# Optimization experiments

Hardware: AMD Instinct MI355X
Metric: run time of the kernel (lower is better)

Reference implementation:

```python
import jax, jax.numpy as jnp
import numpy as np

N, E, H = 50000, 300000, 8  # nodes, edges, FeaStConv heads (PyG default)


def _lin_init(k, fan_in, fan_out):
    k1, k2 = jax.random.split(k)
    s = 1.0 / np.sqrt(fan_in)
    w = jax.random.uniform(k1, (fan_in, fan_out), jnp.float32, -s, s)
    b = jax.random.uniform(k2, (fan_out,), jnp.float32, -s, s)
    return w, b


def _conv_init(k, cin, cout):
    k1, k2 = jax.random.split(k)
    w = jax.random.normal(k1, (cin, H * cout), jnp.float32) * 0.1   # weight
    u = jax.random.normal(k2, (cin, H), jnp.float32) * 0.1          # attention u
    c = jnp.zeros((H,), jnp.float32)                                 # attention bias
    b = jnp.zeros((cout,), jnp.float32)                              # output bias
    return w, u, c, b


def setup_inputs() -> dict:
    key = jax.random.key(0)
    ks = jax.random.split(key, 10)
    x = jax.random.normal(ks[0], (N, 3), jnp.float32)
    src = jax.random.randint(ks[1], (E,), 0, N)
    dst = jax.random.randint(ks[2], (E,), 0, N)
    dst = jnp.where(src == dst, (dst + 1) % N, dst)  # no self loops in raw edge list
    edge_index = jnp.stack([src, dst]).astype(jnp.int64)
    labels = (jax.random.uniform(ks[3], (N, 1)) < 0.1).astype(jnp.float32)
    lin1_w, lin1_b = _lin_init(ks[4], 3, 16)
    c1_w, c1_u, c1_c, c1_b = _conv_init(ks[5], 16, 32)
    c2_w, c2_u, c2_c, c2_b = _conv_init(ks[6], 32, 64)
    c3_w, c3_u, c3_c, c3_b = _conv_init(ks[7], 64, 128)
    lin2_w, lin2_b = _lin_init(ks[8], 128, 1024)
    lin3_w, lin3_b = _lin_init(ks[9], 1024, 1)
    return dict(x=x, edge_index=edge_index, labels=labels,
                lin1_w=lin1_w, lin1_b=lin1_b,
                c1_w=c1_w, c1_u=c1_u, c1_c=c1_c, c1_b=c1_b,
                c2_w=c2_w, c2_u=c2_u, c2_c=c2_c, c2_b=c2_b,
                c3_w=c3_w, c3_u=c3_u, c3_c=c3_c, c3_b=c3_b,
                lin2_w=lin2_w, lin2_b=lin2_b, lin3_w=lin3_w, lin3_b=lin3_b)


def feast_conv(x, src, dst, W, u, c, b):
    """PyG FeaStConv: gather x_i/x_j, head-softmax attention on (x_j - x_i),
    per-edge weighted sum over heads, mean-scatter to destination nodes."""
    n = x.shape[0]
    loop = jnp.arange(n, dtype=src.dtype)
    s = jnp.concatenate([src, loop])  # add self loops (PyG default)
    d = jnp.concatenate([dst, loop])
    xi = x[d]
    xj = x[s]
    q = jax.nn.softmax((xj - xi) @ u + c, axis=-1)           # [E+N, H]
    m = (xj @ W).reshape(xj.shape[0], H, -1)                  # [E+N, H, O]
    msg = jnp.einsum('eh,eho->eo', q, m)                      # [E+N, O]
    agg = jax.ops.segment_sum(msg, d, num_segments=n)
    cnt = jax.ops.segment_sum(jnp.ones_like(d, dtype=msg.dtype), d, num_segments=n)
    return agg / cnt[:, None] + b                             # mean aggregation + bias


def reference(x, edge_index, labels,
              lin1_w, lin1_b,
              c1_w, c1_u, c1_c, c1_b,
              c2_w, c2_u, c2_c, c2_b,
              c3_w, c3_u, c3_c, c3_b,
              lin2_w, lin2_b, lin3_w, lin3_b):
    src, dst = edge_index[0], edge_index[1]
    h = jax.nn.relu(x @ lin1_w + lin1_b)
    h = jax.nn.relu(feast_conv(h, src, dst, c1_w, c1_u, c1_c, c1_b))
    h = jax.nn.relu(feast_conv(h, src, dst, c2_w, c2_u, c2_c, c2_b))
    h = jax.nn.relu(feast_conv(h, src, dst, c3_w, c3_u, c3_c, c3_b))
    h = jax.nn.relu(h @ lin2_w + lin2_b)
    p = jax.nn.sigmoid(h @ lin3_w + lin3_b)                   # [N, 1]
    # generate_weights: class-balanced per-element BCE weights
    n = labels.shape[0]
    pos = jnp.sum(labels)
    neg = n - pos
    w = jnp.where(labels == 1, n / (2.0 * pos), n / (2.0 * neg))
    # torch-style BCE with log clamped at -100
    bce = -(labels * jnp.clip(jnp.log(p), -100.0, None)
            + (1.0 - labels) * jnp.clip(jnp.log(1.0 - p), -100.0, None))
    loss = jnp.mean(w * bce)
    return loss, p
```

## Files before the change

### kernel.cpp

```cpp
#include <hip/hip_runtime.h>
#include <math.h>

#define NN 50000
#define NE 300000

typedef short s8v __attribute__((ext_vector_type(8)));
typedef float f4v __attribute__((ext_vector_type(4)));

__device__ inline unsigned short f2bf(float f) {
    union { float f; unsigned int u; } v; v.f = f;
    unsigned int r = v.u + 0x7FFFu + ((v.u >> 16) & 1u);
    return (unsigned short)(r >> 16);
}

template<int CIN, int O>
__device__ inline void packw_feast_body(const float* __restrict__ W,
                                        unsigned short* __restrict__ wp, int t) {
    constexpr int NS = (8*CIN) / 32;
    int l = t & 63;
    int s = (t >> 6) % NS;
    int ct = t / (64 * NS);
    int c = ct*16 + (l & 15);
    int kk0 = s*32 + (l >> 4) * 8;
    union { unsigned short u[8]; s8v v; } o;
    #pragma unroll
    for (int i = 0; i < 8; ++i) {
        int kk = kk0 + i;
        int h = kk / CIN, k = kk & (CIN - 1);
        o.u[i] = f2bf(W[(size_t)k*(8*O) + h*O + c]);
    }
    *(s8v*)(wp + (size_t)t*8) = o.v;
}

__device__ inline void packw_lin_body(const float* __restrict__ W,
                                      unsigned short* __restrict__ wp, int t) {
    int l = t & 63;
    int s = (t >> 6) & 3;
    int ctg = t >> 8;
    int c = ctg*16 + (l & 15);
    int k0 = s*32 + (l >> 4) * 8;
    union { unsigned short u[8]; s8v v; } o;
    #pragma unroll
    for (int i = 0; i < 8; ++i) o.u[i] = f2bf(W[(size_t)(k0+i)*1024 + c]);
    *(s8v*)(wp + (size_t)t*8) = o.v;
}

__global__ __launch_bounds__(256) void prep_kernel(
        const float* __restrict__ l2w, unsigned short* __restrict__ w2p,
        const float* __restrict__ wf1w, unsigned short* __restrict__ wf1,
        const float* __restrict__ wf2w, unsigned short* __restrict__ wf2,
        const float* __restrict__ wf3w, unsigned short* __restrict__ wf3,
        int* __restrict__ fill, int* __restrict__ fill2,
        float* __restrict__ z, float* __restrict__ scal,
        const float* __restrict__ x, const float* __restrict__ l1w,
        const float* __restrict__ l1b, const float* __restrict__ u1,
        float* __restrict__ h1, float* __restrict__ a) {
    __shared__ float hsh[16][16];
    int b = blockIdx.x;
    int tid = threadIdx.x;
    if (b < 64)  { packw_lin_body(l2w, w2p, b*256 + tid); return; }
    b -= 64;
    if (b < 2)   { packw_feast_body<16,32>(wf1w, wf1, b*256 + tid); return; }
    b -= 2;
    if (b < 8)   { packw_feast_body<32,64>(wf2w, wf2, b*256 + tid); return; }
    b -= 8;
    if (b < 32)  { packw_feast_body<64,128>(wf3w, wf3, b*256 + tid); return; }
    b -= 32;
    if (b < 587) {
        int idx = b*256 + tid;
        if (idx < NN)            fill[idx] = 0;
        else if (idx < 2*NN)     fill2[idx - NN] = 0;
        else if (idx < 3*NN)     z[idx - 2*NN] = 0.f;
        else if (idx < 3*NN+16)  scal[idx - 3*NN] = 0.f;
        return;
    }
    b -= 587;
    int n0 = b * 16;
    int node = n0 + (tid >> 4), col = tid & 15;
    float v = x[node*3+0]*l1w[col] + x[node*3+1]*l1w[16+col]
            + x[node*3+2]*l1w[32+col] + l1b[col];
    v = fmaxf(v, 0.f);
    h1[(size_t)node*16 + col] = v;
    hsh[tid >> 4][col] = v;
    __syncthreads();
    if (tid < 128) {
        int t2 = tid >> 3, h = tid & 7;
        float acc = 0.f;
        #pragma unroll
        for (int k = 0; k < 16; ++k) acc += hsh[t2][k] * u1[k*8 + h];
        a[(size_t)(n0 + t2)*8 + h] = acc;
    }
}

__global__ void hist_kernel(const int* __restrict__ dst, int* __restrict__ cnt) {
    int e = blockIdx.x * 256 + threadIdx.x;
    if (e < NE) atomicAdd(&cnt[dst[e]], 1);
}

__global__ void scan1_kernel(const int* __restrict__ cnt, int* __restrict__ rp,
                             int* __restrict__ bpart) {
    __shared__ int sh[256];
    int tid = threadIdx.x;
    int gid = blockIdx.x * 256 + tid;
    int v = (gid < NN) ? cnt[gid] : 0;
    sh[tid] = v;
    __syncthreads();
    for (int off = 1; off < 256; off <<= 1) {
        int t = (tid >= off) ? sh[tid - off] : 0;
        __syncthreads();
        sh[tid] += t;
        __syncthreads();
    }
    if (gid < NN) rp[gid] = sh[tid] - v;
    if (tid == 255) bpart[blockIdx.x] = sh[tid];
}

__global__ void scanfix_kernel(int* __restrict__ rp, const int* __restrict__ bpart,
                               int nblk) {
    __shared__ int sh[256];
    int tid = threadIdx.x;
    int bx = blockIdx.x;
    sh[tid] = (tid < bx && tid < nblk) ? bpart[tid] : 0;
    __syncthreads();
    for (int off = 128; off; off >>= 1) {
        if (tid < off) sh[tid] += sh[tid + off];
        __syncthreads();
    }
    int add = sh[0];
    int gid = bx * 256 + tid;
    if (gid < NN) rp[gid] += add;
    if (gid == 0) rp[NN] = NE;
}

__global__ void scatter_kernel(const int* __restrict__ src, const int* __restrict__ dst,
                               const int* __restrict__ rp, int* __restrict__ fill,
                               int* __restrict__ ssrc, int* __restrict__ sdst) {
    int e = blockIdx.x * 256 + threadIdx.x;
    if (e >= NE) return;
    int d = dst[e];
    int pos = rp[d] + atomicAdd(&fill[d], 1);
    ssrc[pos] = src[e];
    sdst[pos] = d;
}

__global__ void q_sorted_kernel(const int* __restrict__ ssrc,
                                const int* __restrict__ sdst,
                                const float* __restrict__ a,
                                const float* __restrict__ c,
                                float* __restrict__ qs) {
    int j = blockIdx.x * 256 + threadIdx.x;
    if (j >= NE) return;
    int s = ssrc[j], d = sdst[j];
    const float4* as = (const float4*)(a + (size_t)s*8);
    const float4* ad = (const float4*)(a + (size_t)d*8);
    float4 s0 = as[0], s1 = as[1], d0 = ad[0], d1 = ad[1];
    float lg[8] = { s0.x-d0.x+c[0], s0.y-d0.y+c[1], s0.z-d0.z+c[2], s0.w-d0.w+c[3],
                    s1.x-d1.x+c[4], s1.y-d1.y+c[5], s1.z-d1.z+c[6], s1.w-d1.w+c[7] };
    float m = lg[0];
    #pragma unroll
    for (int h = 1; h < 8; ++h) m = fmaxf(m, lg[h]);
    float sum = 0.f;
    #pragma unroll
    for (int h = 0; h < 8; ++h) { lg[h] = __expf(lg[h]-m); sum += lg[h]; }
    float inv = 1.f / sum;
    float4* qp = (float4*)(qs + (size_t)j*8);
    qp[0] = make_float4(lg[0]*inv, lg[1]*inv, lg[2]*inv, lg[3]*inv);
    qp[1] = make_float4(lg[4]*inv, lg[5]*inv, lg[6]*inv, lg[7]*inv);
}

template<int HPER>
__device__ inline void load_qv(const float* __restrict__ qs, int j, int hg, float* qv) {
    if constexpr (HPER == 2) {
        float2 t = *(const float2*)(qs + (size_t)j*8 + hg*2);
        qv[0] = t.x; qv[1] = t.y;
    } else if constexpr (HPER == 4) {
        float4 t = *(const float4*)(qs + (size_t)j*8 + hg*4);
        qv[0] = t.x; qv[1] = t.y; qv[2] = t.z; qv[3] = t.w;
    } else {
        float4 t0 = *(const float4*)(qs + (size_t)j*8);
        float4 t1 = *(const float4*)(qs + (size_t)j*8 + 4);
        qv[0] = t0.x; qv[1] = t0.y; qv[2] = t0.z; qv[3] = t0.w;
        qv[4] = t1.x; qv[5] = t1.y; qv[6] = t1.z; qv[7] = t1.w;
    }
}

template<int CIN>
__global__ __launch_bounds__(256) void agg_kernel(
        const float* __restrict__ hin, const float* __restrict__ cbias,
        const int* __restrict__ rowptr, const int* __restrict__ ssrc,
        const float* __restrict__ qs, unsigned short* __restrict__ g) {
    constexpr int HPER = CIN / 8;
    constexpr int LG = (CIN == 16) ? 4 : (CIN == 32) ? 5 : 6;
    const int lane = threadIdx.x & 63;
    const int d = blockIdx.x * 4 + (threadIdx.x >> 6);
    const int k = lane & (CIN - 1);
    const int hg = lane >> LG;
    float m = cbias[0];
    #pragma unroll
    for (int h = 1; h < 8; ++h) m = fmaxf(m, cbias[h]);
    float ssum = 0.f;
    #pragma unroll
    for (int h = 0; h < 8; ++h) ssum += __expf(cbias[h] - m);
    float sinv = 1.f / ssum;
    float xd = hin[(size_t)d*CIN + k];
    float acc[HPER];
    #pragma unroll
    for (int i = 0; i < HPER; ++i)
        acc[i] = __expf(cbias[hg*HPER + i] - m) * sinv * xd;
    int j0 = rowptr[d], j1 = rowptr[d+1];
    int j = j0;
    for (; j + 2 <= j1; j += 2) {
        int s0 = ssrc[j], s1 = ssrc[j+1];
        float xv0 = hin[(size_t)s0*CIN + k];
        float xv1 = hin[(size_t)s1*CIN + k];
        float qv0[HPER], qv1[HPER];
        load_qv<HPER>(qs, j, hg, qv0);
        load_qv<HPER>(qs, j+1, hg, qv1);
        #pragma unroll
        for (int i = 0; i < HPER; ++i) acc[i] += qv0[i]*xv0 + qv1[i]*xv1;
    }
    if (j < j1) {
        int s0 = ssrc[j];
        float xv0 = hin[(size_t)s0*CIN + k];
        float qv0[HPER];
        load_qv<HPER>(qs, j, hg, qv0);
        #pragma unroll
        for (int i = 0; i < HPER; ++i) acc[i] += qv0[i]*xv0;
    }
    #pragma unroll
    for (int i = 0; i < HPER; ++i)
        g[(size_t)d*(8*CIN) + (hg*HPER + i)*CIN + k] = f2bf(acc[i]);
}

template<int K, int O, int CH, bool BF16OUT, bool AEPI>
__global__ __launch_bounds__(256) void gemm_feast(
        const unsigned short* __restrict__ g, const unsigned short* __restrict__ wp,
        const int* __restrict__ rowptr, const float* __restrict__ b,
        float* __restrict__ houtf, unsigned short* __restrict__ houtb,
        const float* __restrict__ unext, float* __restrict__ aout) {
    constexpr int NS = K / 32;
    constexpr int NCT = O / 16;
    __shared__ unsigned short bsh[CH*NS*64*8];
    const int l = threadIdx.x & 63;
    const int w = threadIdx.x >> 6;
    const int base = blockIdx.x * 64 + w * 16;
    int arow = base + (l & 15); if (arow >= NN) arow = NN - 1;
    const int koff = (l >> 4) * 8;
    s8v af[NS];
    #pragma unroll
    for (int s = 0; s < NS; ++s)
        af[s] = *(const s8v*)(g + (size_t)arow*K + s*32 + koff);
    float invc[4];
    #pragma unroll
    for (int r = 0; r < 4; ++r) {
        int n = base + (l >> 4)*4 + r; if (n >= NN) n = NN - 1;
        invc[r] = 1.f / (float)(rowptr[n+1] - rowptr[n] + 1);
    }
    float apart[4][8];
    if constexpr (AEPI) {
        #pragma unroll
        for (int r = 0; r < 4; ++r)
            #pragma unroll
            for (int h = 0; h < 8; ++h) apart[r][h] = 0.f;
    }
    #pragma unroll 1
    for (int ct0 = 0; ct0 < NCT; ct0 += CH) {
        __syncthreads();
        const int4* sp = (const int4*)(wp + (size_t)ct0*NS*512);
        int4* dp = (int4*)bsh;
        #pragma unroll 1
        for (int i = threadIdx.x; i < CH*NS*64; i += 256) dp[i] = sp[i];
        __syncthreads();
        #pragma unroll 1
        for (int cc = 0; cc < CH; ++cc) {
            f4v accA = {0.f,0.f,0.f,0.f}, accB = {0.f,0.f,0.f,0.f};
            #pragma unroll
            for (int s = 0; s < NS/2; ++s) {
                s8v bf = *(const s8v*)(bsh + ((size_t)(cc*NS + s)*64 + l)*8);
                accA = __builtin_amdgcn_mfma_f32_16x16x32_bf16(af[s], bf, accA, 0, 0, 0);
            }
            #pragma unroll
            for (int s = NS/2; s < NS; ++s) {
                s8v bf = *(const s8v*)(bsh + ((size_t)(cc*NS + s)*64 + l)*8);
                accB = __builtin_amdgcn_mfma_f32_16x16x32_bf16(af[s], bf, accB, 0, 0, 0);
            }
            int col = (ct0 + cc)*16 + (l & 15);
            float bb = b[col];
            float uv[8];
            if constexpr (AEPI) {
                #pragma unroll
                for (int h = 0; h < 8; ++h) uv[h] = unext[col*8 + h];
            }
            #pragma unroll
            for (int r = 0; r < 4; ++r) {
                int n = base + (l >> 4)*4 + r;
                float v = fmaxf((accA[r]+accB[r])*invc[r] + bb, 0.f);
                if constexpr (AEPI) {
                    #pragma unroll
                    for (int h = 0; h < 8; ++h) apart[r][h] += v * uv[h];
                }
                if (n < NN) {
                    if constexpr (BF16OUT) houtb[(size_t)n*O + col] = f2bf(v);
                    else                   houtf[(size_t)n*O + col] = v;
                }
            }
        }
    }
    if constexpr (AEPI) {
        #pragma unroll
        for (int r = 0; r < 4; ++r)
            #pragma unroll
            for (int h = 0; h < 8; ++h) {
                float v = apart[r][h];
                v += __shfl_xor(v, 1, 64);
                v += __shfl_xor(v, 2, 64);
                v += __shfl_xor(v, 4, 64);
                v += __shfl_xor(v, 8, 64);
                if ((l & 15) == 0) {
                    int n = base + (l >> 4)*4 + r;
                    if (n < NN) aout[(size_t)n*8 + h] = v;
                }
            }
    }
}

__global__ __launch_bounds__(256) void lin23z_kernel(
        const unsigned short* __restrict__ h4b, const unsigned short* __restrict__ w2p,
        const float* __restrict__ b2, const float* __restrict__ w3,
        float* __restrict__ z) {
    const int l = threadIdx.x & 63;
    const int w = threadIdx.x >> 6;
    const int ctg = blockIdx.y;
    const int rowbase = blockIdx.x * 256 + w * 64;
    const int koff = (l >> 4) * 8;
    s8v bf0[4], bf1[4], bf2[4], bf3[4];
    #pragma unroll
    for (int s = 0; s < 4; ++s) {
        bf0[s] = *(const s8v*)(w2p + ((size_t)((ctg*4+0)*4 + s)*64 + l)*8);
        bf1[s] = *(const s8v*)(w2p + ((size_t)((ctg*4+1)*4 + s)*64 + l)*8);
        bf2[s] = *(const s8v*)(w2p + ((size_t)((ctg*4+2)*4 + s)*64 + l)*8);
        bf3[s] = *(const s8v*)(w2p + ((size_t)((ctg*4+3)*4 + s)*64 + l)*8);
    }
    float w3c[4], b2c[4];
    #pragma unroll
    for (int c = 0; c < 4; ++c) {
        int col = (ctg*4 + c)*16 + (l & 15);
        w3c[c] = w3[col]; b2c[c] = b2[col];
    }
    #pragma unroll 1
    for (int t = 0; t < 4; ++t) {
        int base = rowbase + t*16;
        int arow = base + (l & 15); if (arow >= NN) arow = NN - 1;
        s8v af[4];
        #pragma unroll
        for (int s = 0; s < 4; ++s)
            af[s] = *(const s8v*)(h4b + (size_t)arow*128 + s*32 + koff);
        float zp0 = 0.f, zp1 = 0.f, zp2 = 0.f, zp3 = 0.f;
        #pragma unroll
        for (int c = 0; c < 4; ++c) {
            const s8v* bf = (c == 0) ? bf0 : (c == 1) ? bf1 : (c == 2) ? bf2 : bf3;
            f4v accA = {0.f,0.f,0.f,0.f}, accB = {0.f,0.f,0.f,0.f};
            accA = __builtin_amdgcn_mfma_f32_16x16x32_bf16(af[0], bf[0], accA, 0, 0, 0);
            accA = __builtin_amdgcn_mfma_f32_16x16x32_bf16(af[1], bf[1], accA, 0, 0, 0);
            accB = __builtin_amdgcn_mfma_f32_16x16x32_bf16(af[2], bf[2], accB, 0, 0, 0);
            accB = __builtin_amdgcn_mfma_f32_16x16x32_bf16(af[3], bf[3], accB, 0, 0, 0);
            zp0 += fmaxf(accA[0]+accB[0] + b2c[c], 0.f) * w3c[c];
            zp1 += fmaxf(accA[1]+accB[1] + b2c[c], 0.f) * w3c[c];
            zp2 += fmaxf(accA[2]+accB[2] + b2c[c], 0.f) * w3c[c];
            zp3 += fmaxf(accA[3]+accB[3] + b2c[c], 0.f) * w3c[c];
        }
        #pragma unroll
        for (int m = 1; m < 16; m <<= 1) {
            zp0 += __shfl_xor(zp0, m, 64);
            zp1 += __shfl_xor(zp1, m, 64);
            zp2 += __shfl_xor(zp2, m, 64);
            zp3 += __shfl_xor(zp3, m, 64);
        }
        if ((l & 15) == 0) {
            int r0 = base + (l >> 4) * 4;
            if (r0+0 < NN) atomicAdd(&z[r0+0], zp0);
            if (r0+1 < NN) atomicAdd(&z[r0+1], zp1);
            if (r0+2 < NN) atomicAdd(&z[r0+2], zp2);
            if (r0+3 < NN) atomicAdd(&z[r0+3], zp3);
        }
    }
}

__global__ void finish_kernel(const float* __restrict__ labels,
                              const float* __restrict__ z,
                              const float* __restrict__ b3,
                              float* __restrict__ p,
                              float* __restrict__ scal,
                              float* __restrict__ out, int nblk) {
    __shared__ float sh0[256], sh1[256], sh2[256];
    int tid = threadIdx.x;
    int n = blockIdx.x * 256 + tid;
    float pos = 0.f, sp = 0.f, sn = 0.f;
    if (n < NN) {
        float pv = 1.f / (1.f + expf(-(z[n] + b3[0])));
        p[n] = pv;
        float yv = labels[n];
        if (yv == 1.0f) { pos = 1.f; sp = -fmaxf(logf(pv), -100.f); }
        else            { sn = -fmaxf(logf(1.f - pv), -100.f); }
    }
    sh0[tid] = pos; sh1[tid] = sp; sh2[tid] = sn;
    __syncthreads();
    for (int off = 128; off; off >>= 1) {
        if (tid < off) {
            sh0[tid] += sh0[tid+off];
            sh1[tid] += sh1[tid+off];
            sh2[tid] += sh2[tid+off];
        }
        __syncthreads();
    }
    if (tid == 0) {
        atomicAdd(&scal[0], sh0[0]);
        atomicAdd(&scal[1], sh1[0]);
        atomicAdd(&scal[2], sh2[0]);
        __threadfence();
        int t = atomicAdd((int*)&scal[4], 1);
        if (t == nblk - 1) {
            float posT = atomicAdd(&scal[0], 0.f);
            float spT  = atomicAdd(&scal[1], 0.f);
            float snT  = atomicAdd(&scal[2], 0.f);
            out[0] = spT / (2.f*posT) + snT / (2.f*((float)NN - posT));
        }
    }
}

extern "C" void kernel_launch(void* const* d_in, const int* in_sizes, int n_in,
                              void* d_out, int out_size, void* d_ws, size_t ws_size,
                              hipStream_t stream) {
    (void)in_sizes; (void)n_in; (void)out_size; (void)ws_size;
    const float* x   = (const float*)d_in[0];
    const int*   ei  = (const int*)d_in[1];
    const float* labels = (const float*)d_in[2];
    const float* l1w = (const float*)d_in[3];
    const float* l1b = (const float*)d_in[4];
    const float* cw[3] = {(const float*)d_in[5], (const float*)d_in[9],  (const float*)d_in[13]};
    const float* cu[3] = {(const float*)d_in[6], (const float*)d_in[10], (const float*)d_in[14]};
    const float* cc[3] = {(const float*)d_in[7], (const float*)d_in[11], (const float*)d_in[15]};
    const float* cb[3] = {(const float*)d_in[8], (const float*)d_in[12], (const float*)d_in[16]};
    const float* l2w = (const float*)d_in[17];
    const float* l2b = (const float*)d_in[18];
    const float* l3w = (const float*)d_in[19];
    const float* l3b = (const float*)d_in[20];
    const int* srcp = ei;
    const int* dstp = ei + NE;
    float* out = (float*)d_out;

    float* ws = (float*)d_ws;
    size_t off = 0;
    auto alloc = [&](size_t n) { float* p = ws + off; off += (n + 15) & ~(size_t)15; return p; };
    float* hA = alloc((size_t)NN*64);
    float* hB = alloc((size_t)NN*128);
    float* a  = alloc((size_t)NN*8);
    unsigned short* g   = (unsigned short*)alloc((size_t)NN*256);
    unsigned short* w2p = (unsigned short*)alloc(65536);
    unsigned short* wf1 = (unsigned short*)alloc(2048);
    unsigned short* wf2 = (unsigned short*)alloc(8192);
    unsigned short* wf3 = (unsigned short*)alloc(32768);
    float* z    = alloc(NN);
    float* scal = alloc(16);
    int* rowptr = (int*)alloc(50016);
    int* fill   = (int*)alloc(NN);
    int* fill2  = (int*)alloc(NN);
    int* ssrc   = (int*)alloc(NE);
    int* sdst   = (int*)alloc(NE);
    int* bpart  = (int*)alloc(256);
    float* qs1 = hB;
    float* qs2 = hA;
    float* qs3 = hB;
    unsigned short* h4b = (unsigned short*)hB;

    const int SCAN_BLKS = (NN + 255) / 256;
    const int GB = (NN + 63) / 64;
    const int PREP_BLKS = 106 + 587 + NN/16;

    prep_kernel<<<PREP_BLKS, 256, 0, stream>>>(l2w, w2p, cw[0], wf1, cw[1], wf2,
                                               cw[2], wf3, fill, fill2, z, scal,
                                               x, l1w, l1b, cu[0], hA, a);
    hist_kernel<<<(NE+255)/256, 256, 0, stream>>>(dstp, fill);
    scan1_kernel<<<SCAN_BLKS, 256, 0, stream>>>(fill, rowptr, bpart);
    scanfix_kernel<<<SCAN_BLKS, 256, 0, stream>>>(rowptr, bpart, SCAN_BLKS);
    scatter_kernel<<<(NE+255)/256, 256, 0, stream>>>(srcp, dstp, rowptr, fill2, ssrc, sdst);

    q_sorted_kernel<<<(NE+255)/256, 256, 0, stream>>>(ssrc, sdst, a, cc[0], qs1);
    agg_kernel<16><<<NN/4, 256, 0, stream>>>(hA, cc[0], rowptr, ssrc, qs1, g);
    gemm_feast<128,32,2,false,true><<<GB, 256, 0, stream>>>(g, wf1, rowptr, cb[0], hB, nullptr, cu[1], a);

    q_sorted_kernel<<<(NE+255)/256, 256, 0, stream>>>(ssrc, sdst, a, cc[1], qs2);
    agg_kernel<32><<<NN/4, 256, 0, stream>>>(hB, cc[1], rowptr, ssrc, qs2, g);
    gemm_feast<256,64,4,false,true><<<GB, 256, 0, stream>>>(g, wf2, rowptr, cb[1], hA, nullptr, cu[2], a);

    q_sorted_kernel<<<(NE+255)/256, 256, 0, stream>>>(ssrc, sdst, a, cc[2], qs3);
    agg_kernel<64><<<NN/4, 256, 0, stream>>>(hA, cc[2], rowptr, ssrc, qs3, g);
    gemm_feast<512,128,2,true,false><<<GB, 256, 0, stream>>>(g, wf3, rowptr, cb[2], nullptr, h4b, nullptr, nullptr);

    lin23z_kernel<<<dim3((NN+255)/256, 16), 256, 0, stream>>>(h4b, w2p, l2b, l3w, z);
    finish_kernel<<<SCAN_BLKS, 256, 0, stream>>>(labels, z, l3b, out + 1, scal, out, SCAN_BLKS);
}
```

Baseline: 259.4 us.

## Fuse edge softmax into aggregation kernel and store node features as bf16

```diff
diff --git a/kernel.cpp b/kernel.cpp
--- a/kernel.cpp
+++ b/kernel.cpp
@@ -11,6 +11,10 @@
     union { float f; unsigned int u; } v; v.f = f;
     unsigned int r = v.u + 0x7FFFu + ((v.u >> 16) & 1u);
     return (unsigned short)(r >> 16);
+}
+__device__ inline float bf2f(unsigned short u) {
+    union { unsigned int i; float f; } v; v.i = ((unsigned int)u) << 16;
+    return v.f;
 }
 
 template<int CIN, int O>
@@ -54,7 +58,7 @@
         float* __restrict__ z, float* __restrict__ scal,
         const float* __restrict__ x, const float* __restrict__ l1w,
         const float* __restrict__ l1b, const float* __restrict__ u1,
-        float* __restrict__ h1, float* __restrict__ a) {
+        unsigned short* __restrict__ h1, float* __restrict__ a) {
     __shared__ float hsh[16][16];
     int b = blockIdx.x;
     int tid = threadIdx.x;
@@ -80,7 +84,7 @@
     float v = x[node*3+0]*l1w[col] + x[node*3+1]*l1w[16+col]
             + x[node*3+2]*l1w[32+col] + l1b[col];
     v = fmaxf(v, 0.f);
-    h1[(size_t)node*16 + col] = v;
+    h1[(size_t)node*16 + col] = f2bf(v);
     hsh[tid >> 4][col] = v;
     __syncthreads();
     if (tid < 128) {
@@ -134,109 +138,112 @@
 
 __global__ void scatter_kernel(const int* __restrict__ src, const int* __restrict__ dst,
                                const int* __restrict__ rp, int* __restrict__ fill,
-                               int* __restrict__ ssrc, int* __restrict__ sdst) {
+                               int* __restrict__ ssrc) {
     int e = blockIdx.x * 256 + threadIdx.x;
     if (e >= NE) return;
     int d = dst[e];
     int pos = rp[d] + atomicAdd(&fill[d], 1);
     ssrc[pos] = src[e];
-    sdst[pos] = d;
-}
-
-__global__ void q_sorted_kernel(const int* __restrict__ ssrc,
-                                const int* __restrict__ sdst,
-                                const float* __restrict__ a,
-                                const float* __restrict__ c,
-                                float* __restrict__ qs) {
-    int j = blockIdx.x * 256 + threadIdx.x;
-    if (j >= NE) return;
-    int s = ssrc[j], d = sdst[j];
-    const float4* as = (const float4*)(a + (size_t)s*8);
-    const float4* ad = (const float4*)(a + (size_t)d*8);
-    float4 s0 = as[0], s1 = as[1], d0 = ad[0], d1 = ad[1];
-    float lg[8] = { s0.x-d0.x+c[0], s0.y-d0.y+c[1], s0.z-d0.z+c[2], s0.w-d0.w+c[3],
-                    s1.x-d1.x+c[4], s1.y-d1.y+c[5], s1.z-d1.z+c[6], s1.w-d1.w+c[7] };
-    float m = lg[0];
-    #pragma unroll
-    for (int h = 1; h < 8; ++h) m = fmaxf(m, lg[h]);
-    float sum = 0.f;
-    #pragma unroll
-    for (int h = 0; h < 8; ++h) { lg[h] = __expf(lg[h]-m); sum += lg[h]; }
-    float inv = 1.f / sum;
-    float4* qp = (float4*)(qs + (size_t)j*8);
-    qp[0] = make_float4(lg[0]*inv, lg[1]*inv, lg[2]*inv, lg[3]*inv);
-    qp[1] = make_float4(lg[4]*inv, lg[5]*inv, lg[6]*inv, lg[7]*inv);
-}
-
-template<int HPER>
-__device__ inline void load_qv(const float* __restrict__ qs, int j, int hg, float* qv) {
-    if constexpr (HPER == 2) {
-        float2 t = *(const float2*)(qs + (size_t)j*8 + hg*2);
-        qv[0] = t.x; qv[1] = t.y;
-    } else if constexpr (HPER == 4) {
-        float4 t = *(const float4*)(qs + (size_t)j*8 + hg*4);
-        qv[0] = t.x; qv[1] = t.y; qv[2] = t.z; qv[3] = t.w;
-    } else {
-        float4 t0 = *(const float4*)(qs + (size_t)j*8);
-        float4 t1 = *(const float4*)(qs + (size_t)j*8 + 4);
-        qv[0] = t0.x; qv[1] = t0.y; qv[2] = t0.z; qv[3] = t0.w;
-        qv[4] = t1.x; qv[5] = t1.y; qv[6] = t1.z; qv[7] = t1.w;
-    }
 }
 
 template<int CIN>
 __global__ __launch_bounds__(256) void agg_kernel(
-        const float* __restrict__ hin, const float* __restrict__ cbias,
+        const unsigned short* __restrict__ hin, const float* __restrict__ a,
+        const float* __restrict__ cbias,
         const int* __restrict__ rowptr, const int* __restrict__ ssrc,
-        const float* __restrict__ qs, unsigned short* __restrict__ g) {
+        unsigned short* __restrict__ g) {
     constexpr int HPER = CIN / 8;
     constexpr int LG = (CIN == 16) ? 4 : (CIN == 32) ? 5 : 6;
+    __shared__ float qsh[4][64][8];
     const int lane = threadIdx.x & 63;
-    const int d = blockIdx.x * 4 + (threadIdx.x >> 6);
+    const int w = threadIdx.x >> 6;
+    const int d = blockIdx.x * 4 + w;
     const int k = lane & (CIN - 1);
     const int hg = lane >> LG;
-    float m = cbias[0];
-    #pragma unroll
-    for (int h = 1; h < 8; ++h) m = fmaxf(m, cbias[h]);
+    float cc[8], ad[8];
+    #pragma unroll
+    for (int h = 0; h < 8; ++h) { cc[h] = cbias[h]; ad[h] = a[(size_t)d*8 + h]; }
+    float m0 = cc[0];
+    #pragma unroll
+    for (int h = 1; h < 8; ++h) m0 = fmaxf(m0, cc[h]);
     float ssum = 0.f;
     #pragma unroll
-    for (int h = 0; h < 8; ++h) ssum += __expf(cbias[h] - m);
+    for (int h = 0; h < 8; ++h) ssum += __expf(cc[h] - m0);
     float sinv = 1.f / ssum;
-    float xd = hin[(size_t)d*CIN + k];
+    float xd = bf2f(hin[(size_t)d*CIN + k]);
     float acc[HPER];
     #pragma unroll
     for (int i = 0; i < HPER; ++i)
-        acc[i] = __expf(cbias[hg*HPER + i] - m) * sinv * xd;
-    int j0 = rowptr[d], j1 = rowptr[d+1];
-    int j = j0;
-    for (; j + 2 <= j1; j += 2) {
-        int s0 = ssrc[j], s1 = ssrc[j+1];
-        float xv0 = hin[(size_t)s0*CIN + k];
-        float xv1 = hin[(size_t)s1*CIN + k];
-        float qv0[HPER], qv1[HPER];
-        load_qv<HPER>(qs, j, hg, qv0);
-        load_qv<HPER>(qs, j+1, hg, qv1);
-        #pragma unroll
-        for (int i = 0; i < HPER; ++i) acc[i] += qv0[i]*xv0 + qv1[i]*xv1;
-    }
-    if (j < j1) {
-        int s0 = ssrc[j];
-        float xv0 = hin[(size_t)s0*CIN + k];
-        float qv0[HPER];
-        load_qv<HPER>(qs, j, hg, qv0);
-        #pragma unroll
-        for (int i = 0; i < HPER; ++i) acc[i] += qv0[i]*xv0;
+        acc[i] = __expf(cc[hg*HPER + i] - m0) * sinv * xd;
+    const int j0 = rowptr[d], j1 = rowptr[d+1];
+    for (int jb = j0; jb < j1; jb += 64) {
+        int cnt = j1 - jb; if (cnt > 64) cnt = 64;
+        if (lane < cnt) {
+            int s = ssrc[jb + lane];
+            const float4* as = (const float4*)(a + (size_t)s*8);
+            float4 s0 = as[0], s1 = as[1];
+            float lg[8] = { s0.x-ad[0]+cc[0], s0.y-ad[1]+cc[1],
+                            s0.z-ad[2]+cc[2], s0.w-ad[3]+cc[3],
+                            s1.x-ad[4]+cc[4], s1.y-ad[5]+cc[5],
+                            s1.z-ad[6]+cc[6], s1.w-ad[7]+cc[7] };
+            float m = lg[0];
+            #pragma unroll
+            for (int h = 1; h < 8; ++h) m = fmaxf(m, lg[h]);
+            float sum = 0.f;
+            #pragma unroll
+            for (int h = 0; h < 8; ++h) { lg[h] = __expf(lg[h]-m); sum += lg[h]; }
+            float inv = 1.f / sum;
+            float4* qp = (float4*)&qsh[w][lane][0];
+            qp[0] = make_float4(lg[0]*inv, lg[1]*inv, lg[2]*inv, lg[3]*inv);
+            qp[1] = make_float4(lg[4]*inv, lg[5]*inv, lg[6]*inv, lg[7]*inv);
+        }
+        int je = jb + cnt;
+        int j = jb;
+        for (; j + 2 <= je; j += 2) {
+            int s0 = ssrc[j], s1 = ssrc[j+1];
+            float xv0 = bf2f(hin[(size_t)s0*CIN + k]);
+            float xv1 = bf2f(hin[(size_t)s1*CIN + k]);
+            float qv0[HPER], qv1[HPER];
+            if constexpr (HPER == 2) {
+                float2 t0 = *(const float2*)&qsh[w][j-jb][hg*2];
+                float2 t1 = *(const float2*)&qsh[w][j+1-jb][hg*2];
+                qv0[0]=t0.x; qv0[1]=t0.y; qv1[0]=t1.x; qv1[1]=t1.y;
+            } else if constexpr (HPER == 4) {
+                float4 t0 = *(const float4*)&qsh[w][j-jb][hg*4];
+                float4 t1 = *(const float4*)&qsh[w][j+1-jb][hg*4];
+                qv0[0]=t0.x; qv0[1]=t0.y; qv0[2]=t0.z; qv0[3]=t0.w;
+                qv1[0]=t1.x; qv1[1]=t1.y; qv1[2]=t1.z; qv1[3]=t1.w;
+            } else {
+                float4 t0a = *(const float4*)&qsh[w][j-jb][0];
+                float4 t0b = *(const float4*)&qsh[w][j-jb][4];
+                float4 t1a = *(const float4*)&qsh[w][j+1-jb][0];
+                float4 t1b = *(const float4*)&qsh[w][j+1-jb][4];
+                qv0[0]=t0a.x; qv0[1]=t0a.y; qv0[2]=t0a.z; qv0[3]=t0a.w;
+                qv0[4]=t0b.x; qv0[5]=t0b.y; qv0[6]=t0b.z; qv0[7]=t0b.w;
+                qv1[0]=t1a.x; qv1[1]=t1a.y; qv1[2]=t1a.z; qv1[3]=t1a.w;
+                qv1[4]=t1b.x; qv1[5]=t1b.y; qv1[6]=t1b.z; qv1[7]=t1b.w;
+            }
+            #pragma unroll
+            for (int i = 0; i < HPER; ++i) acc[i] += qv0[i]*xv0 + qv1[i]*xv1;
+        }
+        if (j < je) {
+            int s0 = ssrc[j];
+            float xv0 = bf2f(hin[(size_t)s0*CIN + k]);
+            #pragma unroll
+            for (int i = 0; i < HPER; ++i)
+                acc[i] += qsh[w][j-jb][hg*HPER + i] * xv0;
+        }
     }
     #pragma unroll
     for (int i = 0; i < HPER; ++i)
         g[(size_t)d*(8*CIN) + (hg*HPER + i)*CIN + k] = f2bf(acc[i]);
 }
 
-template<int K, int O, int CH, bool BF16OUT, bool AEPI>
+template<int K, int O, int CH, bool AEPI>
 __global__ __launch_bounds__(256) void gemm_feast(
         const unsigned short* __restrict__ g, const unsigned short* __restrict__ wp,
         const int* __restrict__ rowptr, const float* __restrict__ b,
-        float* __restrict__ houtf, unsigned short* __restrict__ houtb,
+        unsigned short* __restrict__ hout,
         const float* __restrict__ unext, float* __restrict__ aout) {
     constexpr int NS = K / 32;
     constexpr int NCT = O / 16;
@@ -299,10 +306,7 @@
                     #pragma unroll
                     for (int h = 0; h < 8; ++h) apart[r][h] += v * uv[h];
                 }
-                if (n < NN) {
-                    if constexpr (BF16OUT) houtb[(size_t)n*O + col] = f2bf(v);
-                    else                   houtf[(size_t)n*O + col] = v;
-                }
+                if (n < NN) hout[(size_t)n*O + col] = f2bf(v);
             }
         }
     }
@@ -452,8 +456,8 @@
     float* ws = (float*)d_ws;
     size_t off = 0;
     auto alloc = [&](size_t n) { float* p = ws + off; off += (n + 15) & ~(size_t)15; return p; };
-    float* hA = alloc((size_t)NN*64);
-    float* hB = alloc((size_t)NN*128);
+    unsigned short* hA = (unsigned short*)alloc((size_t)NN*32);
+    unsigned short* hB = (unsigned short*)alloc((size_t)NN*64);
     float* a  = alloc((size_t)NN*8);
     unsigned short* g   = (unsigned short*)alloc((size_t)NN*256);
     unsigned short* w2p = (unsigned short*)alloc(65536);
@@ -466,12 +470,7 @@
     int* fill   = (int*)alloc(NN);
     int* fill2  = (int*)alloc(NN);
     int* ssrc   = (int*)alloc(NE);
-    int* sdst   = (int*)alloc(NE);
     int* bpart  = (int*)alloc(256);
-    float* qs1 = hB;
-    float* qs2 = hA;
-    float* qs3 = hB;
-    unsigned short* h4b = (unsigned short*)hB;
 
     const int SCAN_BLKS = (NN + 255) / 256;
     const int GB = (NN + 63) / 64;
@@ -483,20 +482,17 @@
     hist_kernel<<<(NE+255)/256, 256, 0, stream>>>(dstp, fill);
     scan1_kernel<<<SCAN_BLKS, 256, 0, stream>>>(fill, rowptr, bpart);
     scanfix_kernel<<<SCAN_BLKS, 256, 0, stream>>>(rowptr, bpart, SCAN_BLKS);
-    scatter_kernel<<<(NE+255)/256, 256, 0, stream>>>(srcp, dstp, rowptr, fill2, ssrc, sdst);
-
-    q_sorted_kernel<<<(NE+255)/256, 256, 0, stream>>>(ssrc, sdst, a, cc[0], qs1);
-    agg_kernel<16><<<NN/4, 256, 0, stream>>>(hA, cc[0], rowptr, ssrc, qs1, g);
-    gemm_feast<128,32,2,false,true><<<GB, 256, 0, stream>>>(g, wf1, rowptr, cb[0], hB, nullptr, cu[1], a);
-
-    q_sorted_kernel<<<(NE+255)/256, 256, 0, stream>>>(ssrc, sdst, a, cc[1], qs2);
-    agg_kernel<32><<<NN/4, 256, 0, stream>>>(hB, cc[1], rowptr, ssrc, qs2, g);
-    gemm_feast<256,64,4,false,true><<<GB, 256, 0, stream>>>(g, wf2, rowptr, cb[1], hA, nullptr, cu[2], a);
-
-    q_sorted_kernel<<<(NE+255)/256, 256, 0, stream>>>(ssrc, sdst, a, cc[2], qs3);
-    agg_kernel<64><<<NN/4, 256, 0, stream>>>(hA, cc[2], rowptr, ssrc, qs3, g);
-    gemm_feast<512,128,2,true,false><<<GB, 256, 0, stream>>>(g, wf3, rowptr, cb[2], nullptr, h4b, nullptr, nullptr);
-
-    lin23z_kernel<<<dim3((NN+255)/256, 16), 256, 0, stream>>>(h4b, w2p, l2b, l3w, z);
+    scatter_kernel<<<(NE+255)/256, 256, 0, stream>>>(srcp, dstp, rowptr, fill2, ssrc);
+
+    agg_kernel<16><<<NN/4, 256, 0, stream>>>(hA, a, cc[0], rowptr, ssrc, g);
+    gemm_feast<128,32,2,true><<<GB, 256, 0, stream>>>(g, wf1, rowptr, cb[0], hB, cu[1], a);
+
+    agg_kernel<32><<<NN/4, 256, 0, stream>>>(hB, a, cc[1], rowptr, ssrc, g);
+    gemm_feast<256,64,4,true><<<GB, 256, 0, stream>>>(g, wf2, rowptr, cb[1], hA, cu[2], a);
+
+    agg_kernel<64><<<NN/4, 256, 0, stream>>>(hA, a, cc[2], rowptr, ssrc, g);
+    gemm_feast<512,128,2,false><<<GB, 256, 0, stream>>>(g, wf3, rowptr, cb[2], hB, nullptr, nullptr);
+
+    lin23z_kernel<<<dim3((NN+255)/256, 16), 256, 0, stream>>>(hB, w2p, l2b, l3w, z);
     finish_kernel<<<SCAN_BLKS, 256, 0, stream>>>(labels, z, l3b, out + 1, scal, out, SCAN_BLKS);
 }
```

After: 246.3 us. 1.05x faster.
